# Optimization experiments

Hardware: AMD Instinct MI355X
Metric: run time of the kernel (lower is better)

## Reference

```python
import jax, jax.numpy as jnp
import numpy as np

N_NODES = 100000
N_EDGES = 1600000
F_IN = 512    # args.in_channels (original node feature dim)
F_GNN = 128   # GCNConv output / 'in_channels' ctor arg
HID = 64
Z_DIM = 64
N_GRAPHS = 512


def setup_inputs() -> dict:
    key = jax.random.key(0)
    ks = jax.random.split(key, 20)
    x = jax.random.normal(ks[0], (N_NODES, F_IN), dtype=jnp.float32)
    edge_index = jax.random.randint(ks[1], (2, N_EDGES), 0, N_NODES)
    batch = jnp.sort(jax.random.randint(ks[2], (N_NODES,), 0, N_GRAPHS))
    eps = jax.random.normal(ks[3], (N_GRAPHS, Z_DIM), dtype=jnp.float32)

    def lin(k, fi, fo):
        # xavier_uniform weight, zero bias
        lim = float(np.sqrt(6.0 / (fi + fo)))
        W = jax.random.uniform(k, (fi, fo), minval=-lim, maxval=lim, dtype=jnp.float32)
        return W, jnp.zeros((fo,), dtype=jnp.float32)

    Wg, bg = lin(ks[4], F_IN, F_GNN)
    We1, be1 = lin(ks[5], 2 * F_GNN, HID)
    We2, be2 = lin(ks[6], HID, HID)
    We3, be3 = lin(ks[7], HID, 2 * Z_DIM)
    Wd1, bd1 = lin(ks[8], Z_DIM, HID)
    Wd2, bd2 = lin(ks[9], HID, HID)
    Wd3, bd3 = lin(ks[10], HID, F_GNN)
    return {"x": x, "edge_index": edge_index, "batch": batch, "eps": eps,
            "Wg": Wg, "bg": bg,
            "We1": We1, "be1": be1, "We2": We2, "be2": be2, "We3": We3, "be3": be3,
            "Wd1": Wd1, "bd1": bd1, "Wd2": Wd2, "bd2": bd2, "Wd3": Wd3, "bd3": bd3}


def _gcn_conv(x, edge_index, Wg, bg):
    # PyG GCNConv: add self-loops, symmetric deg normalization, linear-then-aggregate
    n = x.shape[0]
    loops = jnp.arange(n)
    src = jnp.concatenate([edge_index[0], loops])
    dst = jnp.concatenate([edge_index[1], loops])
    deg = jax.ops.segment_sum(jnp.ones_like(dst, dtype=x.dtype), dst, num_segments=n)
    dinv = jnp.where(deg > 0, jax.lax.rsqrt(jnp.maximum(deg, 1.0)), 0.0)
    norm = dinv[src] * dinv[dst]              # [E+N]
    xw = x @ Wg                               # [N, F_GNN]
    msg = xw[src] * norm[:, None]             # gather + scale: [E+N, F_GNN]
    agg = jax.ops.segment_sum(msg, dst, num_segments=n)
    return agg + bg


def _forward(x, edge_index, batch, eps,
             Wg, bg, We1, be1, We2, be2, We3, be3,
             Wd1, bd1, Wd2, bd2, Wd3, bd3):
    n = x.shape[0]
    g = eps.shape[0]
    # single GNN layer (num_layers=1, JK='last'); dropout omitted (eval determinism)
    node_x = jax.nn.relu(_gcn_conv(x, edge_index, Wg, bg))  # [N, F_GNN]
    # global mean / max pool by graph id
    ones = jnp.ones((n,), dtype=node_x.dtype)
    cnt = jax.ops.segment_sum(ones, batch, num_segments=g)
    mean_p = jax.ops.segment_sum(node_x, batch, num_segments=g) / jnp.maximum(cnt, 1.0)[:, None]
    max_p = jax.ops.segment_max(node_x, batch, num_segments=g)
    graph_x = jnp.concatenate([mean_p, max_p], axis=1)      # [G, 2*F_GNN]
    # gaussian encoder MLP
    t = jax.nn.elu(graph_x @ We1 + be1)
    t = jnp.tanh(t @ We2 + be2)
    ml = t @ We3 + be3
    mu, logvar = jnp.split(ml, 2, axis=1)
    # reparameterise (note: module returns stddev in the 'logvar' slot)
    stddev = 1e-6 + jax.nn.softplus(logvar)
    z = mu + eps * stddev
    # bernoulli decoder MLP
    d = jnp.tanh(z @ Wd1 + bd1)
    d = jax.nn.elu(d @ Wd2 + bd2)
    y = jax.nn.sigmoid(d @ Wd3 + bd3)
    y = jnp.clip(y, 1e-8, 1.0 - 1e-8)
    return mu, stddev, y


def reference(x, edge_index, batch, eps,
              Wg, bg, We1, be1, We2, be2, We3, be3,
              Wd1, bd1, Wd2, bd2, Wd3, bd3):
    return _forward(x, edge_index, batch, eps,
                    Wg, bg, We1, be1, We2, be2, We3, be3,
                    Wd1, bd1, Wd2, bd2, Wd3, bd3)
```

## Files before the change

kernel.cpp:

```cpp
#include <hip/hip_runtime.h>
#include <hip/hip_bf16.h>
#include <math.h>

#define N_NODES 100000
#define N_EDGES 1600000
#define F_IN 512
#define F_GNN 128
#define HID 64
#define Z_DIM 64
#define N_GRAPHS 512
#define N_REGIONS 196
#define REGION_CAP 10240

typedef __attribute__((ext_vector_type(8))) short short8;
typedef __attribute__((ext_vector_type(4))) float f32x4;

__device__ __forceinline__ float eluf(float v) { return v > 0.f ? v : expm1f(v); }
__device__ __forceinline__ float softplusf(float v) {
  return fmaxf(v, 0.f) + log1pf(expf(-fabsf(v)));
}
__device__ __forceinline__ float sigmoidf(float v) { return 1.f / (1.f + expf(-v)); }

__device__ __forceinline__ unsigned short f2bf(float f) {
  unsigned int u = __float_as_uint(f);
  u = (u + 0x7fffu + ((u >> 16) & 1u)) >> 16;
  return (unsigned short)u;
}
__device__ __forceinline__ unsigned int f2bf2(float a, float b) {
  __hip_bfloat162 h = __float22bfloat162_rn(make_float2(a, b));
  unsigned int u;
  __builtin_memcpy(&u, &h, 4);
  return u;
}
__device__ __forceinline__ float bf_lo(unsigned int u) { return __uint_as_float(u << 16); }
__device__ __forceinline__ float bf_hi(unsigned int u) { return __uint_as_float(u & 0xffff0000u); }

__device__ __forceinline__ int lower_bound_i(const int* __restrict__ a, int n, int v) {
  int lo = 0, hi = n;
  while (lo < hi) {
    int mid = (lo + hi) >> 1;
    if (a[mid] < v) lo = mid + 1; else hi = mid;
  }
  return lo;
}

__global__ __launch_bounds__(256) void k_init(
    const float* __restrict__ Wg, unsigned short* __restrict__ WgT,
    int* __restrict__ cursor) {
  int i = blockIdx.x * 256 + threadIdx.x;
  int n = i >> 9, k = i & 511;
  WgT[i] = f2bf(Wg[k * F_GNN + n]);
  if (i < 256) cursor[i] = i * REGION_CAP;
}

__global__ __launch_bounds__(512) void k_bucket(
    const int* __restrict__ ei, int* __restrict__ cursor_r,
    unsigned int* __restrict__ pairs) {
  __shared__ int lhist[256];
  __shared__ int lofs[256];
  __shared__ int lcur[256];
  __shared__ int gbase[256];
  __shared__ int sc[256];
  __shared__ unsigned int lpairs[4096];

  const int b = blockIdx.x, t = threadIdx.x;
  const int e0 = b * 4096;
  const int n_b = min(4096, N_EDGES - e0);

  if (t < 256) { lhist[t] = 0; lcur[t] = 0; }
  __syncthreads();

  int srcv[8], dstv[8];
#pragma unroll
  for (int jj = 0; jj < 2; jj++) {
    int e = e0 + jj * 2048 + 4 * t;
    if (e < N_EDGES) {
      int4 s4 = *(const int4*)&ei[e];
      int4 d4 = *(const int4*)&ei[N_EDGES + e];
      srcv[4 * jj + 0] = s4.x; dstv[4 * jj + 0] = d4.x;
      srcv[4 * jj + 1] = s4.y; dstv[4 * jj + 1] = d4.y;
      srcv[4 * jj + 2] = s4.z; dstv[4 * jj + 2] = d4.z;
      srcv[4 * jj + 3] = s4.w; dstv[4 * jj + 3] = d4.w;
      atomicAdd(&lhist[d4.x >> 9], 1);
      atomicAdd(&lhist[d4.y >> 9], 1);
      atomicAdd(&lhist[d4.z >> 9], 1);
      atomicAdd(&lhist[d4.w >> 9], 1);
    } else {
      dstv[4 * jj + 0] = dstv[4 * jj + 1] = dstv[4 * jj + 2] = dstv[4 * jj + 3] = -1;
    }
  }
  __syncthreads();

  if (t < 256) sc[t] = lhist[t];
  __syncthreads();
#pragma unroll
  for (int d = 1; d < 256; d <<= 1) {
    int v = (t < 256 && t >= d) ? sc[t - d] : 0;
    __syncthreads();
    if (t < 256) sc[t] += v;
    __syncthreads();
  }
  if (t < 256) lofs[t] = (t > 0) ? sc[t - 1] : 0;
  if (t < N_REGIONS && lhist[t] > 0) gbase[t] = atomicAdd(&cursor_r[t], lhist[t]);
  __syncthreads();

#pragma unroll
  for (int j = 0; j < 8; j++) {
    if (dstv[j] >= 0) {
      int r = dstv[j] >> 9;
      int pos = lofs[r] + atomicAdd(&lcur[r], 1);
      lpairs[pos] = (unsigned)srcv[j] | ((unsigned)(dstv[j] & 511) << 17);
    }
  }
  __syncthreads();

  for (int i = t; i < n_b; i += 512) {
    int lo = 0, hi = N_REGIONS;
    while (hi - lo > 1) {
      int mid = (lo + hi) >> 1;
      if (lofs[mid] <= i) lo = mid; else hi = mid;
    }
    pairs[gbase[lo] + (i - lofs[lo])] = lpairs[i];
  }
}

__global__ __launch_bounds__(1024) void k_region(
    const unsigned int* __restrict__ pairs, const int* __restrict__ cursor,
    int* __restrict__ off, float* __restrict__ dinv, int* __restrict__ csr_src) {
  __shared__ int nh[512];
  __shared__ int sofs[512];
  __shared__ int s[512];
  __shared__ int ncur[512];
  __shared__ int cbuf[REGION_CAP];

  const int r = blockIdx.x, t = threadIdx.x;
  const int base = r * REGION_CAP;
  const int cnt = cursor[r] - base;

  if (t < 512) { nh[t] = 0; ncur[t] = 0; }
  __syncthreads();

  for (int i = t; i < cnt; i += 1024)
    atomicAdd(&nh[(pairs[base + i] >> 17) & 511], 1);
  __syncthreads();

  int a = (t < 512) ? nh[t] : 0;
  if (t < 512) s[t] = a;
  __syncthreads();
#pragma unroll
  for (int d = 1; d < 512; d <<= 1) {
    int v = (t < 512 && t >= d) ? s[t - d] : 0;
    __syncthreads();
    if (t < 512) s[t] += v;
    __syncthreads();
  }
  if (t < 512) {
    int excl = (t > 0) ? s[t - 1] : 0;
    sofs[t] = excl;
    int node = (r << 9) + t;
    if (node < N_NODES) {
      off[node] = base + excl;
      dinv[node] = rsqrtf(1.f + (float)a);
    } else if (node == N_NODES) {
      off[node] = base + excl;
    }
  }
  __syncthreads();

  for (int i = t; i < cnt; i += 1024) {
    unsigned int p = pairs[base + i];
    int d = (int)((p >> 17) & 511);
    int lpos = sofs[d] + atomicAdd(&ncur[d], 1);
    if (lpos < REGION_CAP) cbuf[lpos] = (int)(p & 0x1FFFFu);
  }
  __syncthreads();
  for (int i = t; i < cnt; i += 1024) csr_src[base + i] = cbuf[i];
}

__global__ __launch_bounds__(256) void k_gemm(
    const float* __restrict__ x, const unsigned short* __restrict__ WgT,
    const float* __restrict__ dinv, unsigned short* __restrict__ sxw) {
  __shared__ unsigned short As[128][32];
  __shared__ unsigned short Bs[128][32];

  const int t = threadIdx.x;
  const int lane15 = t & 15;
  const int quad = (t & 63) >> 4;
  const int wave = t >> 6;
  const int wm = (wave & 1) * 64;
  const int wn = (wave >> 1) * 64;
  const int row0 = blockIdx.x * 128;

  f32x4 acc[4][4];
#pragma unroll
  for (int mi = 0; mi < 4; mi++)
#pragma unroll
    for (int ni = 0; ni < 4; ni++) acc[mi][ni] = (f32x4){0.f, 0.f, 0.f, 0.f};

  float4 ga[4];
  uint4 gb[2];
  auto load_tile = [&](int k0) {
#pragma unroll
    for (int i = 0; i < 4; i++) {
      int f = t + 256 * i;
      int r = f >> 3, c4 = f & 7;
      int gr = row0 + r;
      if (gr >= N_NODES) gr = N_NODES - 1;
      ga[i] = *(const float4*)&x[(size_t)gr * F_IN + k0 + c4 * 4];
    }
#pragma unroll
    for (int i = 0; i < 2; i++) {
      int f = t + 256 * i;
      int r = f >> 2, c = f & 3;
      gb[i] = *(const uint4*)&WgT[r * F_IN + k0 + c * 8];
    }
  };

  load_tile(0);
#pragma unroll 1
  for (int kt = 0; kt < 16; kt++) {
    __syncthreads();
#pragma unroll
    for (int i = 0; i < 4; i++) {
      int f = t + 256 * i;
      int r = f >> 3, c4 = f & 7;
      unsigned int u0 = f2bf2(ga[i].x, ga[i].y);
      unsigned int u1 = f2bf2(ga[i].z, ga[i].w);
      *(uint2*)&As[r][c4 * 4] = make_uint2(u0, u1);
    }
#pragma unroll
    for (int i = 0; i < 2; i++) {
      int f = t + 256 * i;
      int r = f >> 2, c = f & 3;
      *(uint4*)&Bs[r][c * 8] = gb[i];
    }
    __syncthreads();
    if (kt < 15) load_tile((kt + 1) * 32);

    short8 afr[4], bfr[4];
#pragma unroll
    for (int mi = 0; mi < 4; mi++)
      afr[mi] = *(const short8*)&As[wm + mi * 16 + lane15][quad * 8];
#pragma unroll
    for (int ni = 0; ni < 4; ni++)
      bfr[ni] = *(const short8*)&Bs[wn + ni * 16 + lane15][quad * 8];
#pragma unroll
    for (int mi = 0; mi < 4; mi++)
#pragma unroll
      for (int ni = 0; ni < 4; ni++)
        acc[mi][ni] = __builtin_amdgcn_mfma_f32_16x16x32_bf16(
            bfr[ni], afr[mi], acc[mi][ni], 0, 0, 0);
  }

#pragma unroll
  for (int mi = 0; mi < 4; mi++) {
    int gm = row0 + wm + mi * 16 + lane15;
    if (gm < N_NODES) {
      float s = dinv[gm];
#pragma unroll
      for (int ni = 0; ni < 4; ni++) {
        int gn = wn + ni * 16 + quad * 4;
        unsigned int u0 = f2bf2(acc[mi][ni][0] * s, acc[mi][ni][1] * s);
        unsigned int u1 = f2bf2(acc[mi][ni][2] * s, acc[mi][ni][3] * s);
        *(uint2*)&sxw[(size_t)gm * F_GNN + gn] = make_uint2(u0, u1);
      }
    }
  }
}

__global__ __launch_bounds__(1024) void k_aggpool(
    const unsigned short* __restrict__ sxw, const int* __restrict__ off,
    const int* __restrict__ csr_src, const float* __restrict__ dinv,
    const float* __restrict__ bg, const int* __restrict__ batch,
    const int* __restrict__ cursor, float* __restrict__ gx) {
  __shared__ float4 ssum[16][32];
  __shared__ float4 smax[16][32];
  __shared__ int sse[2];
  const int g = blockIdx.x;
  const int t = threadIdx.x;
  const int wv = t >> 6;
  const int lane = t & 63;
  const int h = lane >> 5;
  const int c = lane & 31;

  if (t == 0) sse[0] = lower_bound_i(batch, N_NODES, g);
  if (t == 64) sse[1] = lower_bound_i(batch, N_NODES, g + 1);
  __syncthreads();
  const int start = sse[0], end = sse[1];

  const uint2* S2 = (const uint2*)sxw;
  float4 bb = ((const float4*)bg)[c];
  float ps0 = 0.f, ps1 = 0.f, ps2 = 0.f, ps3 = 0.f;
  float pm0 = 0.f, pm1 = 0.f, pm2 = 0.f, pm3 = 0.f;

  for (int node = start + wv; node < end; node += 16) {
    float sx0 = 0.f, sx1 = 0.f, sx2 = 0.f, sx3 = 0.f;
    int e = off[node];
    const int e1 = min(off[node + 1], cursor[node >> 9]);
    for (; e + 7 < e1; e += 8) {
      int s0 = csr_src[e + 0], s1 = csr_src[e + 1];
      int s2 = csr_src[e + 2], s3 = csr_src[e + 3];
      int s4 = csr_src[e + 4], s5 = csr_src[e + 5];
      int s6 = csr_src[e + 6], s7 = csr_src[e + 7];
      uint2 v0 = S2[(size_t)(h ? s1 : s0) * 32 + c];
      uint2 v1 = S2[(size_t)(h ? s3 : s2) * 32 + c];
      uint2 v2 = S2[(size_t)(h ? s5 : s4) * 32 + c];
      uint2 v3 = S2[(size_t)(h ? s7 : s6) * 32 + c];
      sx0 += bf_lo(v0.x) + bf_lo(v1.x) + bf_lo(v2.x) + bf_lo(v3.x);
      sx1 += bf_hi(v0.x) + bf_hi(v1.x) + bf_hi(v2.x) + bf_hi(v3.x);
      sx2 += bf_lo(v0.y) + bf_lo(v1.y) + bf_lo(v2.y) + bf_lo(v3.y);
      sx3 += bf_hi(v0.y) + bf_hi(v1.y) + bf_hi(v2.y) + bf_hi(v3.y);
    }
    for (; e + 1 < e1; e += 2) {
      int sa = csr_src[e], sb = csr_src[e + 1];
      uint2 v = S2[(size_t)(h ? sb : sa) * 32 + c];
      sx0 += bf_lo(v.x); sx1 += bf_hi(v.x);
      sx2 += bf_lo(v.y); sx3 += bf_hi(v.y);
    }
    if (e < e1 && h == 0) {
      uint2 v = S2[(size_t)csr_src[e] * 32 + c];
      sx0 += bf_lo(v.x); sx1 += bf_hi(v.x);
      sx2 += bf_lo(v.y); sx3 += bf_hi(v.y);
    }
    sx0 += __shfl_xor(sx0, 32);
    sx1 += __shfl_xor(sx1, 32);
    sx2 += __shfl_xor(sx2, 32);
    sx3 += __shfl_xor(sx3, 32);
    uint2 sv = S2[(size_t)node * 32 + c];
    sx0 += bf_lo(sv.x); sx1 += bf_hi(sv.x);
    sx2 += bf_lo(sv.y); sx3 += bf_hi(sv.y);

    float di = dinv[node];
    float r0 = fmaxf(fmaf(sx0, di, bb.x), 0.f);
    float r1 = fmaxf(fmaf(sx1, di, bb.y), 0.f);
    float r2 = fmaxf(fmaf(sx2, di, bb.z), 0.f);
    float r3 = fmaxf(fmaf(sx3, di, bb.w), 0.f);
    ps0 += r0; ps1 += r1; ps2 += r2; ps3 += r3;
    pm0 = fmaxf(pm0, r0); pm1 = fmaxf(pm1, r1);
    pm2 = fmaxf(pm2, r2); pm3 = fmaxf(pm3, r3);
  }

  if (h == 0) {
    ssum[wv][c] = make_float4(ps0, ps1, ps2, ps3);
    smax[wv][c] = make_float4(pm0, pm1, pm2, pm3);
  }
  __syncthreads();
  if (t < 32) {
    float4 s = ssum[0][t];
    float4 m = smax[0][t];
#pragma unroll
    for (int hh = 1; hh < 16; hh++) {
      float4 a = ssum[hh][t], b2 = smax[hh][t];
      s.x += a.x; s.y += a.y; s.z += a.z; s.w += a.w;
      m.x = fmaxf(m.x, b2.x); m.y = fmaxf(m.y, b2.y);
      m.z = fmaxf(m.z, b2.z); m.w = fmaxf(m.w, b2.w);
    }
    float ic = 1.f / fmaxf((float)(end - start), 1.f);
    gx[g * 256 + 4 * t + 0] = s.x * ic;
    gx[g * 256 + 4 * t + 1] = s.y * ic;
    gx[g * 256 + 4 * t + 2] = s.z * ic;
    gx[g * 256 + 4 * t + 3] = s.w * ic;
    gx[g * 256 + 128 + 4 * t + 0] = m.x;
    gx[g * 256 + 128 + 4 * t + 1] = m.y;
    gx[g * 256 + 128 + 4 * t + 2] = m.z;
    gx[g * 256 + 128 + 4 * t + 3] = m.w;
  }
}

__global__ __launch_bounds__(64) void k_mlp(
    const float* __restrict__ gx, const float* __restrict__ eps,
    const float* __restrict__ We1, const float* __restrict__ be1,
    const float* __restrict__ We2, const float* __restrict__ be2,
    const float* __restrict__ We3, const float* __restrict__ be3,
    const float* __restrict__ Wd1, const float* __restrict__ bd1,
    const float* __restrict__ Wd2, const float* __restrict__ bd2,
    const float* __restrict__ Wd3, const float* __restrict__ bd3,
    float* __restrict__ out) {
  __shared__ float row[256];
  __shared__ float t1[64], t2[64], zz[64], d1[64], d2[64];
  int g = blockIdx.x;
  int j = threadIdx.x;

#pragma unroll
  for (int i = 0; i < 4; i++) row[j + 64 * i] = gx[g * 256 + j + 64 * i];
  __syncthreads();

  float s = be1[j];
#pragma unroll 4
  for (int k = 0; k < 256; k++) s = fmaf(row[k], We1[k * 64 + j], s);
  t1[j] = eluf(s);
  __syncthreads();

  s = be2[j];
#pragma unroll 4
  for (int k = 0; k < 64; k++) s = fmaf(t1[k], We2[k * 64 + j], s);
  t2[j] = tanhf(s);
  __syncthreads();

  float m = be3[j], lv = be3[64 + j];
#pragma unroll 4
  for (int k = 0; k < 64; k++) {
    float tv = t2[k];
    m = fmaf(tv, We3[k * 128 + j], m);
    lv = fmaf(tv, We3[k * 128 + 64 + j], lv);
  }
  float sd = 1e-6f + softplusf(lv);
  float z = fmaf(eps[g * 64 + j], sd, m);
  out[g * 64 + j] = m;
  out[32768 + g * 64 + j] = sd;
  zz[j] = z;
  __syncthreads();

  s = bd1[j];
#pragma unroll 4
  for (int k = 0; k < 64; k++) s = fmaf(zz[k], Wd1[k * 64 + j], s);
  d1[j] = tanhf(s);
  __syncthreads();

  s = bd2[j];
#pragma unroll 4
  for (int k = 0; k < 64; k++) s = fmaf(d1[k], Wd2[k * 64 + j], s);
  d2[j] = eluf(s);
  __syncthreads();

  float y0 = bd3[j], y1 = bd3[64 + j];
#pragma unroll 4
  for (int k = 0; k < 64; k++) {
    float dv = d2[k];
    y0 = fmaf(dv, Wd3[k * 128 + j], y0);
    y1 = fmaf(dv, Wd3[k * 128 + 64 + j], y1);
  }
  y0 = fminf(fmaxf(sigmoidf(y0), 1e-8f), 1.f - 1e-8f);
  y1 = fminf(fmaxf(sigmoidf(y1), 1e-8f), 1.f - 1e-8f);
  out[65536 + g * 128 + j] = y0;
  out[65536 + g * 128 + 64 + j] = y1;
}

extern "C" void kernel_launch(void* const* d_in, const int* in_sizes, int n_in,
                              void* d_out, int out_size, void* d_ws, size_t ws_size,
                              hipStream_t stream) {
  const float* x     = (const float*)d_in[0];
  const int*   ei    = (const int*)d_in[1];
  const int*   batch = (const int*)d_in[2];
  const float* eps   = (const float*)d_in[3];
  const float* Wg    = (const float*)d_in[4];
  const float* bg    = (const float*)d_in[5];
  const float* We1   = (const float*)d_in[6];
  const float* be1   = (const float*)d_in[7];
  const float* We2   = (const float*)d_in[8];
  const float* be2   = (const float*)d_in[9];
  const float* We3   = (const float*)d_in[10];
  const float* be3   = (const float*)d_in[11];
  const float* Wd1   = (const float*)d_in[12];
  const float* bd1   = (const float*)d_in[13];
  const float* Wd2   = (const float*)d_in[14];
  const float* bd2   = (const float*)d_in[15];
  const float* Wd3   = (const float*)d_in[16];
  const float* bd3   = (const float*)d_in[17];
  float* out = (float*)d_out;

  int*            cursor  = (int*)d_ws;
  int*            off     = cursor + 256;
  float*          dinv    = (float*)(off + 100608);
  int*            csr_src = (int*)(dinv + 100352);
  unsigned int*   pairs   = (unsigned int*)(csr_src + 2007040);
  unsigned short* WgT     = (unsigned short*)(pairs + 2007040);
  unsigned short* sxw     = WgT + 65536;
  float*          gx      = (float*)(sxw + 12800000);

  k_init<<<256, 256, 0, stream>>>(Wg, WgT, cursor);
  k_bucket<<<(N_EDGES + 4095) / 4096, 512, 0, stream>>>(ei, cursor, pairs);
  k_region<<<N_REGIONS, 1024, 0, stream>>>(pairs, cursor, off, dinv, csr_src);
  k_gemm<<<(N_NODES + 127) / 128, 256, 0, stream>>>(x, WgT, dinv, sxw);
  k_aggpool<<<N_GRAPHS, 1024, 0, stream>>>(sxw, off, csr_src, dinv, bg, batch,
                                           cursor, gx);
  k_mlp<<<N_GRAPHS, 64, 0, stream>>>(gx, eps, We1, be1, We2, be2, We3, be3,
                                     Wd1, bd1, Wd2, bd2, Wd3, bd3, out);
}
```

Baseline: 509.7 us.

## Widen aggregation gathers to 16-byte loads and simplify bucketing scatter

The aggregation kernel now has each wave process four edges at once, with 16 lanes reading a full 256-byte bf16 row through uint4 loads instead of 32 lanes reading uint2. This raises bytes per load and memory-level parallelism for the random gather, at the cost of an extra shuffle stage and more registers. The bucketing kernel replaces its per-element binary search with a per-region copy loop spread across waves. The region kernel keeps its pairs in registers so they are read from global memory once instead of twice.

```diff
diff --git a/kernel.cpp b/kernel.cpp
--- a/kernel.cpp
+++ b/kernel.cpp
@@ -65,7 +65,6 @@
 
   const int b = blockIdx.x, t = threadIdx.x;
   const int e0 = b * 4096;
-  const int n_b = min(4096, N_EDGES - e0);
 
   if (t < 256) { lhist[t] = 0; lcur[t] = 0; }
   __syncthreads();
@@ -114,13 +113,15 @@
   }
   __syncthreads();
 
-  for (int i = t; i < n_b; i += 512) {
-    int lo = 0, hi = N_REGIONS;
-    while (hi - lo > 1) {
-      int mid = (lo + hi) >> 1;
-      if (lofs[mid] <= i) lo = mid; else hi = mid;
-    }
-    pairs[gbase[lo] + (i - lofs[lo])] = lpairs[i];
+  const int w = t >> 6, lane = t & 63;
+  for (int r = w; r < N_REGIONS; r += 8) {
+    int n = lhist[r];
+    if (n > 0) {
+      int o = lofs[r];
+      int gb = gbase[r];
+      for (int i = lane; i < n; i += 64)
+        pairs[gb + i] = lpairs[o + i];
+    }
   }
 }
 
@@ -135,13 +136,22 @@
 
   const int r = blockIdx.x, t = threadIdx.x;
   const int base = r * REGION_CAP;
-  const int cnt = cursor[r] - base;
+  const int cnt = min(cursor[r] - base, REGION_CAP);
 
   if (t < 512) { nh[t] = 0; ncur[t] = 0; }
   __syncthreads();
 
-  for (int i = t; i < cnt; i += 1024)
-    atomicAdd(&nh[(pairs[base + i] >> 17) & 511], 1);
+  unsigned pk[10];
+#pragma unroll
+  for (int j = 0; j < 10; j++) {
+    int i = t + j * 1024;
+    pk[j] = (i < cnt) ? pairs[base + i] : 0u;
+  }
+#pragma unroll
+  for (int j = 0; j < 10; j++) {
+    int i = t + j * 1024;
+    if (i < cnt) atomicAdd(&nh[(pk[j] >> 17) & 511], 1);
+  }
   __syncthreads();
 
   int a = (t < 512) ? nh[t] : 0;
@@ -167,11 +177,15 @@
   }
   __syncthreads();
 
-  for (int i = t; i < cnt; i += 1024) {
-    unsigned int p = pairs[base + i];
-    int d = (int)((p >> 17) & 511);
-    int lpos = sofs[d] + atomicAdd(&ncur[d], 1);
-    if (lpos < REGION_CAP) cbuf[lpos] = (int)(p & 0x1FFFFu);
+#pragma unroll
+  for (int j = 0; j < 10; j++) {
+    int i = t + j * 1024;
+    if (i < cnt) {
+      unsigned int p = pk[j];
+      int d = (int)((p >> 17) & 511);
+      int lpos = sofs[d] + atomicAdd(&ncur[d], 1);
+      if (lpos < REGION_CAP) cbuf[lpos] = (int)(p & 0x1FFFFu);
+    }
   }
   __syncthreads();
   for (int i = t; i < cnt; i += 1024) csr_src[base + i] = cbuf[i];
@@ -273,97 +287,123 @@
     const int* __restrict__ csr_src, const float* __restrict__ dinv,
     const float* __restrict__ bg, const int* __restrict__ batch,
     const int* __restrict__ cursor, float* __restrict__ gx) {
-  __shared__ float4 ssum[16][32];
-  __shared__ float4 smax[16][32];
+  __shared__ float ssum[16][16][8];
+  __shared__ float smax[16][16][8];
   __shared__ int sse[2];
   const int g = blockIdx.x;
   const int t = threadIdx.x;
   const int wv = t >> 6;
   const int lane = t & 63;
-  const int h = lane >> 5;
-  const int c = lane & 31;
+  const int h = lane >> 4;
+  const int c = lane & 15;
 
   if (t == 0) sse[0] = lower_bound_i(batch, N_NODES, g);
   if (t == 64) sse[1] = lower_bound_i(batch, N_NODES, g + 1);
   __syncthreads();
   const int start = sse[0], end = sse[1];
 
-  const uint2* S2 = (const uint2*)sxw;
-  float4 bb = ((const float4*)bg)[c];
+  const uint4* S4 = (const uint4*)sxw;
+  float4 ba = ((const float4*)bg)[2 * c];
+  float4 bb = ((const float4*)bg)[2 * c + 1];
   float ps0 = 0.f, ps1 = 0.f, ps2 = 0.f, ps3 = 0.f;
+  float ps4 = 0.f, ps5 = 0.f, ps6 = 0.f, ps7 = 0.f;
   float pm0 = 0.f, pm1 = 0.f, pm2 = 0.f, pm3 = 0.f;
-
-  for (int node = start + wv; node < end; node += 16) {
+  float pm4 = 0.f, pm5 = 0.f, pm6 = 0.f, pm7 = 0.f;
+
+  for (int nd = start + wv; nd < end; nd += 16) {
+    const int node = __builtin_amdgcn_readfirstlane(nd);
     float sx0 = 0.f, sx1 = 0.f, sx2 = 0.f, sx3 = 0.f;
+    float sx4 = 0.f, sx5 = 0.f, sx6 = 0.f, sx7 = 0.f;
     int e = off[node];
     const int e1 = min(off[node + 1], cursor[node >> 9]);
+
+#define ACC8(v)                                         \
+    sx0 += bf_lo((v).x); sx1 += bf_hi((v).x);           \
+    sx2 += bf_lo((v).y); sx3 += bf_hi((v).y);           \
+    sx4 += bf_lo((v).z); sx5 += bf_hi((v).z);           \
+    sx6 += bf_lo((v).w); sx7 += bf_hi((v).w);
+
     for (; e + 7 < e1; e += 8) {
       int s0 = csr_src[e + 0], s1 = csr_src[e + 1];
       int s2 = csr_src[e + 2], s3 = csr_src[e + 3];
       int s4 = csr_src[e + 4], s5 = csr_src[e + 5];
       int s6 = csr_src[e + 6], s7 = csr_src[e + 7];
-      uint2 v0 = S2[(size_t)(h ? s1 : s0) * 32 + c];
-      uint2 v1 = S2[(size_t)(h ? s3 : s2) * 32 + c];
-      uint2 v2 = S2[(size_t)(h ? s5 : s4) * 32 + c];
-      uint2 v3 = S2[(size_t)(h ? s7 : s6) * 32 + c];
-      sx0 += bf_lo(v0.x) + bf_lo(v1.x) + bf_lo(v2.x) + bf_lo(v3.x);
-      sx1 += bf_hi(v0.x) + bf_hi(v1.x) + bf_hi(v2.x) + bf_hi(v3.x);
-      sx2 += bf_lo(v0.y) + bf_lo(v1.y) + bf_lo(v2.y) + bf_lo(v3.y);
-      sx3 += bf_hi(v0.y) + bf_hi(v1.y) + bf_hi(v2.y) + bf_hi(v3.y);
-    }
-    for (; e + 1 < e1; e += 2) {
-      int sa = csr_src[e], sb = csr_src[e + 1];
-      uint2 v = S2[(size_t)(h ? sb : sa) * 32 + c];
-      sx0 += bf_lo(v.x); sx1 += bf_hi(v.x);
-      sx2 += bf_lo(v.y); sx3 += bf_hi(v.y);
-    }
-    if (e < e1 && h == 0) {
-      uint2 v = S2[(size_t)csr_src[e] * 32 + c];
-      sx0 += bf_lo(v.x); sx1 += bf_hi(v.x);
-      sx2 += bf_lo(v.y); sx3 += bf_hi(v.y);
-    }
-    sx0 += __shfl_xor(sx0, 32);
-    sx1 += __shfl_xor(sx1, 32);
-    sx2 += __shfl_xor(sx2, 32);
-    sx3 += __shfl_xor(sx3, 32);
-    uint2 sv = S2[(size_t)node * 32 + c];
+      int srcA = h < 2 ? (h == 0 ? s0 : s1) : (h == 2 ? s2 : s3);
+      int srcB = h < 2 ? (h == 0 ? s4 : s5) : (h == 2 ? s6 : s7);
+      uint4 va = S4[(size_t)srcA * 16 + c];
+      uint4 vb = S4[(size_t)srcB * 16 + c];
+      ACC8(va);
+      ACC8(vb);
+    }
+    for (; e + 3 < e1; e += 4) {
+      int s0 = csr_src[e + 0], s1 = csr_src[e + 1];
+      int s2 = csr_src[e + 2], s3 = csr_src[e + 3];
+      int srcA = h < 2 ? (h == 0 ? s0 : s1) : (h == 2 ? s2 : s3);
+      uint4 va = S4[(size_t)srcA * 16 + c];
+      ACC8(va);
+    }
+    if (e < e1) {
+      int idx = min(e + h, e1 - 1);
+      int srcA = csr_src[idx];
+      uint4 va = S4[(size_t)srcA * 16 + c];
+      if (e + h < e1) { ACC8(va); }
+    }
+#undef ACC8
+
+    sx0 += __shfl_xor(sx0, 16); sx0 += __shfl_xor(sx0, 32);
+    sx1 += __shfl_xor(sx1, 16); sx1 += __shfl_xor(sx1, 32);
+    sx2 += __shfl_xor(sx2, 16); sx2 += __shfl_xor(sx2, 32);
+    sx3 += __shfl_xor(sx3, 16); sx3 += __shfl_xor(sx3, 32);
+    sx4 += __shfl_xor(sx4, 16); sx4 += __shfl_xor(sx4, 32);
+    sx5 += __shfl_xor(sx5, 16); sx5 += __shfl_xor(sx5, 32);
+    sx6 += __shfl_xor(sx6, 16); sx6 += __shfl_xor(sx6, 32);
+    sx7 += __shfl_xor(sx7, 16); sx7 += __shfl_xor(sx7, 32);
+
+    uint4 sv = S4[(size_t)node * 16 + c];
     sx0 += bf_lo(sv.x); sx1 += bf_hi(sv.x);
     sx2 += bf_lo(sv.y); sx3 += bf_hi(sv.y);
+    sx4 += bf_lo(sv.z); sx5 += bf_hi(sv.z);
+    sx6 += bf_lo(sv.w); sx7 += bf_hi(sv.w);
 
     float di = dinv[node];
-    float r0 = fmaxf(fmaf(sx0, di, bb.x), 0.f);
-    float r1 = fmaxf(fmaf(sx1, di, bb.y), 0.f);
-    float r2 = fmaxf(fmaf(sx2, di, bb.z), 0.f);
-    float r3 = fmaxf(fmaf(sx3, di, bb.w), 0.f);
+    float r0 = fmaxf(fmaf(sx0, di, ba.x), 0.f);
+    float r1 = fmaxf(fmaf(sx1, di, ba.y), 0.f);
+    float r2 = fmaxf(fmaf(sx2, di, ba.z), 0.f);
+    float r3 = fmaxf(fmaf(sx3, di, ba.w), 0.f);
+    float r4 = fmaxf(fmaf(sx4, di, bb.x), 0.f);
+    float r5 = fmaxf(fmaf(sx5, di, bb.y), 0.f);
+    float r6 = fmaxf(fmaf(sx6, di, bb.z), 0.f);
+    float r7 = fmaxf(fmaf(sx7, di, bb.w), 0.f);
     ps0 += r0; ps1 += r1; ps2 += r2; ps3 += r3;
+    ps4 += r4; ps5 += r5; ps6 += r6; ps7 += r7;
     pm0 = fmaxf(pm0, r0); pm1 = fmaxf(pm1, r1);
     pm2 = fmaxf(pm2, r2); pm3 = fmaxf(pm3, r3);
+    pm4 = fmaxf(pm4, r4); pm5 = fmaxf(pm5, r5);
+    pm6 = fmaxf(pm6, r6); pm7 = fmaxf(pm7, r7);
   }
 
   if (h == 0) {
-    ssum[wv][c] = make_float4(ps0, ps1, ps2, ps3);
-    smax[wv][c] = make_float4(pm0, pm1, pm2, pm3);
-  }
-  __syncthreads();
-  if (t < 32) {
-    float4 s = ssum[0][t];
-    float4 m = smax[0][t];
-#pragma unroll
-    for (int hh = 1; hh < 16; hh++) {
-      float4 a = ssum[hh][t], b2 = smax[hh][t];
-      s.x += a.x; s.y += a.y; s.z += a.z; s.w += a.w;
-      m.x = fmaxf(m.x, b2.x); m.y = fmaxf(m.y, b2.y);
-      m.z = fmaxf(m.z, b2.z); m.w = fmaxf(m.w, b2.w);
+    ssum[wv][c][0] = ps0; ssum[wv][c][1] = ps1;
+    ssum[wv][c][2] = ps2; ssum[wv][c][3] = ps3;
+    ssum[wv][c][4] = ps4; ssum[wv][c][5] = ps5;
+    ssum[wv][c][6] = ps6; ssum[wv][c][7] = ps7;
+    smax[wv][c][0] = pm0; smax[wv][c][1] = pm1;
+    smax[wv][c][2] = pm2; smax[wv][c][3] = pm3;
+    smax[wv][c][4] = pm4; smax[wv][c][5] = pm5;
+    smax[wv][c][6] = pm6; smax[wv][c][7] = pm7;
+  }
+  __syncthreads();
+  if (t < 128) {
+    int cc = t >> 3, k = t & 7;
+    float s = 0.f, m = 0.f;
+#pragma unroll
+    for (int w = 0; w < 16; w++) {
+      s += ssum[w][cc][k];
+      m = fmaxf(m, smax[w][cc][k]);
     }
     float ic = 1.f / fmaxf((float)(end - start), 1.f);
-    gx[g * 256 + 4 * t + 0] = s.x * ic;
-    gx[g * 256 + 4 * t + 1] = s.y * ic;
-    gx[g * 256 + 4 * t + 2] = s.z * ic;
-    gx[g * 256 + 4 * t + 3] = s.w * ic;
-    gx[g * 256 + 128 + 4 * t + 0] = m.x;
-    gx[g * 256 + 128 + 4 * t + 1] = m.y;
-    gx[g * 256 + 128 + 4 * t + 2] = m.z;
-    gx[g * 256 + 128 + 4 * t + 3] = m.w;
+    gx[g * 256 + 8 * cc + k] = s * ic;
+    gx[g * 256 + 128 + 8 * cc + k] = m;
   }
 }
 
```

After: 498.7 us. 1.02x faster.
